# Kernel optimization log

Hardware: AMD Instinct MI355X
Metric: run time of the kernel (lower is better)

## Reference

```python
import jax, jax.numpy as jnp
import numpy as np

RADIUS = 0.5
NEG_INF = -jnp.inf


def setup_inputs() -> dict:
    key = jax.random.key(0)
    ks = jax.random.split(key, 10)
    N_q, N_o, pos_dim, latent_dim = 2048, 2048, 3, 64
    enc_dim = 3 * pos_dim  # q_pos, o_pos, rel
    inp = {
        "h_obs": jax.random.normal(ks[0], (N_o, latent_dim), dtype=jnp.float32),
        "x_obs": jax.random.normal(ks[1], (N_o, latent_dim), dtype=jnp.float32),
        "pos_obs": jax.random.uniform(ks[2], (N_o, pos_dim), dtype=jnp.float32),
        "pos_query": jax.random.uniform(ks[3], (N_q, pos_dim), dtype=jnp.float32),
        # kernel_mlp: Linear(enc_dim->latent) + ReLU + Linear(latent->1)
        "W1": jax.random.normal(ks[4], (enc_dim, latent_dim), dtype=jnp.float32) / np.sqrt(enc_dim),
        "b1": jnp.zeros((latent_dim,), dtype=jnp.float32),
        "W2": jax.random.normal(ks[5], (latent_dim, 1), dtype=jnp.float32) / np.sqrt(latent_dim),
        "b2": jnp.zeros((1,), dtype=jnp.float32),
        # value_proj: Linear(latent->latent)
        "Wv": jax.random.normal(ks[6], (latent_dim, latent_dim), dtype=jnp.float32) / np.sqrt(latent_dim),
        "bv": jnp.zeros((latent_dim,), dtype=jnp.float32),
    }
    return inp


def reference(h_obs, x_obs, pos_obs, pos_query, W1, b1, W2, b2, Wv, bv):
    # rel: [N_q, N_o, pos_dim]
    rel = pos_query[:, None, :] - pos_obs[None, :, :]
    N_q, N_o, _ = rel.shape
    pos_q_exp = jnp.broadcast_to(pos_query[:, None, :], rel.shape)
    pos_o_exp = jnp.broadcast_to(pos_obs[None, :, :], rel.shape)
    kernel_input = jnp.concatenate([pos_q_exp, pos_o_exp, rel], axis=-1)  # [N_q, N_o, 3*pos_dim]
    # small pointwise MLP over all pairs
    hidden = jax.nn.relu(jnp.einsum('qoe,el->qol', kernel_input, W1) + b1)  # [N_q, N_o, latent]
    logits = jnp.einsum('qol,lk->qok', hidden, W2)[..., 0] + b2[0]          # [N_q, N_o]
    # radius mask
    dist = jnp.linalg.norm(rel, axis=-1)
    logits = jnp.where(dist > RADIUS, NEG_INF, logits)
    # softmax over observations (dim=1)
    weights = jax.nn.softmax(logits, axis=1)  # [N_q, N_o]
    v = h_obs @ Wv + bv                        # [N_o, latent]
    h_query = weights @ v                      # [N_q, latent]
    return h_query
```

## Files before the change

kernel.cpp:

```cpp
#include <hip/hip_runtime.h>

#define NQ 2048
#define NO 2048
#define NOC 32

constexpr size_t OFF_PH = 0;
constexpr size_t OFF_PS = (size_t)NOC * NQ * 64;

typedef _Float16 h2t __attribute__((ext_vector_type(2)));

#if defined(__has_builtin)
#if __has_builtin(__builtin_amdgcn_fdot2)
#define FDOT2(a, b, c) __builtin_amdgcn_fdot2((a), (b), (c), false)
#endif
#endif
#ifndef FDOT2
#define FDOT2(a, b, c) ((c) + (float)(a)[0] * (float)(b)[0] + (float)(a)[1] * (float)(b)[1])
#endif

__device__ __forceinline__ float pack2(float a, float b) {
    return __builtin_bit_cast(float, __builtin_amdgcn_cvt_pkrtz(a, b));
}
__device__ __forceinline__ h2t ash2(float f) {
    return __builtin_bit_cast(h2t, f);
}
__device__ __forceinline__ h2t relu2(h2t x) {
    return __builtin_elementwise_max(x, (h2t)(_Float16)0);
}

__global__ __launch_bounds__(256, 4) void gano_main(
    const float* __restrict__ h_obs,
    const float* __restrict__ pos_obs,
    const float* __restrict__ pos_query,
    const float* __restrict__ W1,
    const float* __restrict__ b1,
    const float* __restrict__ W2,
    float* __restrict__ Ph,
    float* __restrict__ Ps)
{
    __shared__ __align__(16) float tl2[8 * 64 * 4];
    __shared__ __align__(16) float ue[64 * 64];
    __shared__ float w1q[3 * 64];
    __shared__ float w1o[3 * 64];
    __shared__ float b1l[64];
    __shared__ __align__(16) float w2h[32];
    __shared__ float po[3 * 64];
    __shared__ float sbuf[4 * 64];

    const int tid  = threadIdx.x;
    const int lane = tid & 63;
    const int wave = __builtin_amdgcn_readfirstlane(tid >> 6);
    const int qg = blockIdx.x >> 5;
    const int oc = blockIdx.x & 31;
    const int obase = oc * 64;
    const int q = qg * 64 + lane;

    if (tid < 64) {
        float w6 = W1[6 * 64 + tid], w7 = W1[7 * 64 + tid], w8 = W1[8 * 64 + tid];
        w1q[0 * 64 + tid] = W1[0 * 64 + tid] + w6;
        w1q[1 * 64 + tid] = W1[1 * 64 + tid] + w7;
        w1q[2 * 64 + tid] = W1[2 * 64 + tid] + w8;
        w1o[0 * 64 + tid] = W1[3 * 64 + tid] - w6;
        w1o[1 * 64 + tid] = W1[4 * 64 + tid] - w7;
        w1o[2 * 64 + tid] = W1[5 * 64 + tid] - w8;
        b1l[tid] = b1[tid];
    }
    if (tid >= 64 && tid < 96) {
        int p = tid - 64;
        w2h[p] = pack2(W2[2 * p], W2[2 * p + 1]);
    }
    float pq0 = pos_query[q * 3 + 0];
    float pq1 = pos_query[q * 3 + 1];
    float pq2 = pos_query[q * 3 + 2];
    float po0 = pos_obs[(obase + lane) * 3 + 0];
    float po1 = pos_obs[(obase + lane) * 3 + 1];
    float po2 = pos_obs[(obase + lane) * 3 + 2];
    if (wave == 0) { po[lane] = po0; po[64 + lane] = po1; po[128 + lane] = po2; }
    __syncthreads();

    {
        float tv[16];
#pragma unroll
        for (int j = 0; j < 16; ++j) {
            int l = wave * 16 + j;
            tv[j] = po0 * w1o[l] + po1 * w1o[64 + l] + po2 * w1o[128 + l];
        }
        float4 p0, p1;
        p0.x = pack2(tv[0], tv[1]);  p0.y = pack2(tv[2], tv[3]);
        p0.z = pack2(tv[4], tv[5]);  p0.w = pack2(tv[6], tv[7]);
        p1.x = pack2(tv[8], tv[9]);  p1.y = pack2(tv[10], tv[11]);
        p1.z = pack2(tv[12], tv[13]); p1.w = pack2(tv[14], tv[15]);
        *(float4*)(tl2 + (size_t)((2 * wave) * 64 + lane) * 4) = p0;
        *(float4*)(tl2 + (size_t)((2 * wave + 1) * 64 + lane) * 4) = p1;
    }
#pragma unroll
    for (int k = 0; k < 2; ++k) {
        const int c = wave * 2 + k;
        float uv[8];
#pragma unroll
        for (int d = 0; d < 8; ++d) {
            int l = c * 8 + d;
            uv[d] = b1l[l] + pq0 * w1q[l] + pq1 * w1q[64 + l] + pq2 * w1q[128 + l];
        }
        float4 up;
        up.x = pack2(uv[0], uv[1]); up.y = pack2(uv[2], uv[3]);
        up.z = pack2(uv[4], uv[5]); up.w = pack2(uv[6], uv[7]);
        *(float4*)(ue + (size_t)(c * 64 + lane) * 4) = up;
    }
    __syncthreads();

    float lg[16];
#pragma unroll
    for (int o = 0; o < 16; ++o) lg[o] = 0.f;
    const int ow = wave * 16;
#pragma unroll
    for (int c = 0; c < 8; ++c) {
        float4 u4 = *(const float4*)(ue + (size_t)(c * 64 + lane) * 4);
        float4 w4 = *(const float4*)(w2h + c * 4);
        h2t u0 = ash2(u4.x), u1 = ash2(u4.y), u2 = ash2(u4.z), u3 = ash2(u4.w);
        h2t w0 = ash2(w4.x), w1 = ash2(w4.y), w2 = ash2(w4.z), w3 = ash2(w4.w);
        const float4* tr = (const float4*)tl2 + (c * 64 + ow);
#pragma unroll
        for (int j = 0; j < 16; ++j) {
            float4 t4 = tr[j];
            h2t a0 = relu2(u0 + ash2(t4.x));
            h2t a1 = relu2(u1 + ash2(t4.y));
            h2t a2 = relu2(u2 + ash2(t4.z));
            h2t a3 = relu2(u3 + ash2(t4.w));
            float acc = lg[j];
            acc = FDOT2(a0, w0, acc);
            acc = FDOT2(a1, w1, acc);
            acc = FDOT2(a2, w2, acc);
            acc = FDOT2(a3, w3, acc);
            lg[j] = acc;
        }
    }
    float e[16], spart = 0.f;
#pragma unroll
    for (int o = 0; o < 16; ++o) {
        float d0 = pq0 - po[ow + o];
        float d1 = pq1 - po[64 + ow + o];
        float d2 = pq2 - po[128 + ow + o];
        float dd = d0 * d0 + d1 * d1 + d2 * d2;
        float ev = (dd > 0.25f) ? 0.f : __expf(lg[o]);
        e[o] = ev; spart += ev;
    }
    __syncthreads();
#pragma unroll
    for (int o = 0; o < 16; ++o) ue[(size_t)(ow + o) * 64 + lane] = e[o];
    sbuf[wave * 64 + lane] = spart;
    __syncthreads();

    float h0 = 0.f, h1 = 0.f, h2 = 0.f, h3 = 0.f, h4 = 0.f, h5 = 0.f, h6 = 0.f, h7 = 0.f;
    float h8 = 0.f, h9 = 0.f, hA = 0.f, hB = 0.f, hC = 0.f, hD = 0.f, hE = 0.f, hF = 0.f;
    const float* vb = h_obs + (size_t)obase * 64 + ow;
#pragma unroll 4
    for (int o = 0; o < 64; ++o) {
        float eo = ue[(size_t)o * 64 + lane];
        const float4* vr = (const float4*)(vb + (size_t)o * 64);
        float4 v0 = vr[0], v1 = vr[1], v2 = vr[2], v3 = vr[3];
        h0 += eo * v0.x; h1 += eo * v0.y; h2 += eo * v0.z; h3 += eo * v0.w;
        h4 += eo * v1.x; h5 += eo * v1.y; h6 += eo * v1.z; h7 += eo * v1.w;
        h8 += eo * v2.x; h9 += eo * v2.y; hA += eo * v2.z; hB += eo * v2.w;
        hC += eo * v3.x; hD += eo * v3.y; hE += eo * v3.z; hF += eo * v3.w;
    }

    float* hp = Ph + ((size_t)oc * NQ + (size_t)qg * 64 + lane) * 64 + ow;
    ((float4*)hp)[0] = make_float4(h0, h1, h2, h3);
    ((float4*)hp)[1] = make_float4(h4, h5, h6, h7);
    ((float4*)hp)[2] = make_float4(h8, h9, hA, hB);
    ((float4*)hp)[3] = make_float4(hC, hD, hE, hF);
    if (wave == 0) {
        float s = sbuf[lane] + sbuf[64 + lane] + sbuf[128 + lane] + sbuf[192 + lane];
        Ps[(size_t)oc * NQ + (size_t)qg * 64 + lane] = s;
    }
}

__global__ __launch_bounds__(256, 2) void gano_comb(
    const float* __restrict__ Ph,
    const float* __restrict__ Ps,
    const float* __restrict__ Wv,
    const float* __restrict__ bv,
    float* __restrict__ out)
{
    __shared__ __align__(16) float wv[64 * 64];
    __shared__ __align__(16) float g[4 * 68];
    const int tid  = threadIdx.x;
    const int lane = tid & 63;
    const int wave = tid >> 6;
    const int q0 = blockIdx.x * 4;
    {
        const float4* src = (const float4*)Wv;
        float4* dst = (float4*)wv;
#pragma unroll
        for (int k = 0; k < 4; ++k) dst[tid + k * 256] = src[tid + k * 256];
    }
    {
        const int qi = wave, k = lane;
        float acc = 0.f;
#pragma unroll
        for (int c = 0; c < NOC; ++c)
            acc += Ph[((size_t)c * NQ + q0 + qi) * 64 + k];
        g[qi * 68 + k] = acc;
        if (k == 0) {
            float ss = 0.f;
#pragma unroll
            for (int c = 0; c < NOC; ++c) ss += Ps[(size_t)c * NQ + q0 + qi];
            g[qi * 68 + 64] = ss;
        }
    }
    __syncthreads();
    const float* gq = g + wave * 68;
    float inv = 1.0f / gq[64];
    float a0 = 0.f, a1 = 0.f, a2 = 0.f, a3 = 0.f;
#pragma unroll
    for (int kb = 0; kb < 16; ++kb) {
        float4 g4 = *(const float4*)(gq + kb * 4);
        a0 += g4.x * wv[(kb * 4 + 0) * 64 + lane];
        a1 += g4.y * wv[(kb * 4 + 1) * 64 + lane];
        a2 += g4.z * wv[(kb * 4 + 2) * 64 + lane];
        a3 += g4.w * wv[(kb * 4 + 3) * 64 + lane];
    }
    out[(size_t)(q0 + wave) * 64 + lane] = ((a0 + a1) + (a2 + a3)) * inv + bv[lane];
}

extern "C" void kernel_launch(void* const* d_in, const int* in_sizes, int n_in,
                              void* d_out, int out_size, void* d_ws, size_t ws_size,
                              hipStream_t stream) {
    const float* h_obs     = (const float*)d_in[0];
    const float* pos_obs   = (const float*)d_in[2];
    const float* pos_query = (const float*)d_in[3];
    const float* W1        = (const float*)d_in[4];
    const float* b1        = (const float*)d_in[5];
    const float* W2        = (const float*)d_in[6];
    const float* Wv        = (const float*)d_in[8];
    const float* bv        = (const float*)d_in[9];
    float* ws  = (float*)d_ws;
    float* out = (float*)d_out;

    gano_main<<<dim3(1024), dim3(256), 0, stream>>>(h_obs, pos_obs, pos_query, W1, b1, W2,
                                                    ws + OFF_PH, ws + OFF_PS);
    gano_comb<<<dim3(NQ / 4), dim3(256), 0, stream>>>(ws + OFF_PH, ws + OFF_PS, Wv, bv, out);
}
```

Before: 104.6 us.

## Stage h_obs as packed fp16 pairs in LDS and use fdot2 for weighted sum

Each block now loads its 64 h_obs rows once into shared memory, converting pairs of observations into packed half2 values. The softmax numerators are packed the same way. The weighted accumulation then runs as 32 fdot2 steps reading LDS instead of 64 fp32 FMA steps reading global memory. The outer logit loop is also no longer fully unrolled. This cuts global traffic and FMA count but lowers the precision of the values and weights to fp16, and the added LDS may reduce occupancy.

```diff
diff --git a/kernel.cpp b/kernel.cpp
--- a/kernel.cpp
+++ b/kernel.cpp
@@ -39,7 +39,8 @@
     float* __restrict__ Ps)
 {
     __shared__ __align__(16) float tl2[8 * 64 * 4];
-    __shared__ __align__(16) float ue[64 * 64];
+    __shared__ __align__(16) float ue[8 * 64 * 4];
+    __shared__ __align__(16) float hpk[32 * 68];
     __shared__ float w1q[3 * 64];
     __shared__ float w1o[3 * 64];
     __shared__ float b1l[64];
@@ -76,6 +77,22 @@
     float po1 = pos_obs[(obase + lane) * 3 + 1];
     float po2 = pos_obs[(obase + lane) * 3 + 2];
     if (wave == 0) { po[lane] = po0; po[64 + lane] = po1; po[128 + lane] = po2; }
+
+    {
+        const int p  = tid >> 3;
+        const int l0 = (tid & 7) * 8;
+        const float* r0 = h_obs + (size_t)(obase + 2 * p) * 64 + l0;
+        const float* r1 = r0 + 64;
+        float4 a0 = ((const float4*)r0)[0], a1 = ((const float4*)r0)[1];
+        float4 c0 = ((const float4*)r1)[0], c1 = ((const float4*)r1)[1];
+        float4 o0, o1;
+        o0.x = pack2(a0.x, c0.x); o0.y = pack2(a0.y, c0.y);
+        o0.z = pack2(a0.z, c0.z); o0.w = pack2(a0.w, c0.w);
+        o1.x = pack2(a1.x, c1.x); o1.y = pack2(a1.y, c1.y);
+        o1.z = pack2(a1.z, c1.z); o1.w = pack2(a1.w, c1.w);
+        *(float4*)(hpk + p * 68 + l0)     = o0;
+        *(float4*)(hpk + p * 68 + l0 + 4) = o1;
+    }
     __syncthreads();
 
     {
@@ -113,7 +130,6 @@
 #pragma unroll
     for (int o = 0; o < 16; ++o) lg[o] = 0.f;
     const int ow = wave * 16;
-#pragma unroll
     for (int c = 0; c < 8; ++c) {
         float4 u4 = *(const float4*)(ue + (size_t)(c * 64 + lane) * 4);
         float4 w4 = *(const float4*)(w2h + c * 4);
@@ -135,37 +151,50 @@
             lg[j] = acc;
         }
     }
-    float e[16], spart = 0.f;
-#pragma unroll
-    for (int o = 0; o < 16; ++o) {
-        float d0 = pq0 - po[ow + o];
-        float d1 = pq1 - po[64 + ow + o];
-        float d2 = pq2 - po[128 + ow + o];
-        float dd = d0 * d0 + d1 * d1 + d2 * d2;
-        float ev = (dd > 0.25f) ? 0.f : __expf(lg[o]);
-        e[o] = ev; spart += ev;
-    }
-    __syncthreads();
-#pragma unroll
-    for (int o = 0; o < 16; ++o) ue[(size_t)(ow + o) * 64 + lane] = e[o];
+    float pk[8], spart = 0.f;
+#pragma unroll
+    for (int j = 0; j < 8; ++j) {
+        float ev[2];
+#pragma unroll
+        for (int i = 0; i < 2; ++i) {
+            int o = 2 * j + i;
+            float d0 = pq0 - po[ow + o];
+            float d1 = pq1 - po[64 + ow + o];
+            float d2 = pq2 - po[128 + ow + o];
+            float dd = d0 * d0 + d1 * d1 + d2 * d2;
+            ev[i] = (dd > 0.25f) ? 0.f : __expf(lg[o]);
+        }
+        float pkj = pack2(ev[0], ev[1]);
+        h2t pp = ash2(pkj);
+        spart += (float)pp[0] + (float)pp[1];
+        pk[j] = pkj;
+    }
+    __syncthreads();
+#pragma unroll
+    for (int j = 0; j < 8; ++j)
+        ue[(size_t)(wave * 8 + j) * 64 + lane] = pk[j];
     sbuf[wave * 64 + lane] = spart;
     __syncthreads();
 
     float h0 = 0.f, h1 = 0.f, h2 = 0.f, h3 = 0.f, h4 = 0.f, h5 = 0.f, h6 = 0.f, h7 = 0.f;
     float h8 = 0.f, h9 = 0.f, hA = 0.f, hB = 0.f, hC = 0.f, hD = 0.f, hE = 0.f, hF = 0.f;
-    const float* vb = h_obs + (size_t)obase * 64 + ow;
+    const int lw = wave * 16;
 #pragma unroll 4
-    for (int o = 0; o < 64; ++o) {
-        float eo = ue[(size_t)o * 64 + lane];
-        const float4* vr = (const float4*)(vb + (size_t)o * 64);
-        float4 v0 = vr[0], v1 = vr[1], v2 = vr[2], v3 = vr[3];
-        h0 += eo * v0.x; h1 += eo * v0.y; h2 += eo * v0.z; h3 += eo * v0.w;
-        h4 += eo * v1.x; h5 += eo * v1.y; h6 += eo * v1.z; h7 += eo * v1.w;
-        h8 += eo * v2.x; h9 += eo * v2.y; hA += eo * v2.z; hB += eo * v2.w;
-        hC += eo * v3.x; hD += eo * v3.y; hE += eo * v3.z; hF += eo * v3.w;
-    }
-
-    float* hp = Ph + ((size_t)oc * NQ + (size_t)qg * 64 + lane) * 64 + ow;
+    for (int p = 0; p < 32; ++p) {
+        h2t e2 = ash2(ue[(size_t)p * 64 + lane]);
+        const float4* hr = (const float4*)(hpk + p * 68 + lw);
+        float4 x0 = hr[0], x1 = hr[1], x2 = hr[2], x3 = hr[3];
+        h0 = FDOT2(e2, ash2(x0.x), h0); h1 = FDOT2(e2, ash2(x0.y), h1);
+        h2 = FDOT2(e2, ash2(x0.z), h2); h3 = FDOT2(e2, ash2(x0.w), h3);
+        h4 = FDOT2(e2, ash2(x1.x), h4); h5 = FDOT2(e2, ash2(x1.y), h5);
+        h6 = FDOT2(e2, ash2(x1.z), h6); h7 = FDOT2(e2, ash2(x1.w), h7);
+        h8 = FDOT2(e2, ash2(x2.x), h8); h9 = FDOT2(e2, ash2(x2.y), h9);
+        hA = FDOT2(e2, ash2(x2.z), hA); hB = FDOT2(e2, ash2(x2.w), hB);
+        hC = FDOT2(e2, ash2(x3.x), hC); hD = FDOT2(e2, ash2(x3.y), hD);
+        hE = FDOT2(e2, ash2(x3.z), hE); hF = FDOT2(e2, ash2(x3.w), hF);
+    }
+
+    float* hp = Ph + ((size_t)oc * NQ + (size_t)qg * 64 + lane) * 64 + lw;
     ((float4*)hp)[0] = make_float4(h0, h1, h2, h3);
     ((float4*)hp)[1] = make_float4(h4, h5, h6, h7);
     ((float4*)hp)[2] = make_float4(h8, h9, hA, hB);
```

New measurement: 105.1 us. No clear change (+0.5%).
